# Kernel tuning notes

Measured on AMD Instinct MI355X. Metric: run time of the kernel, lower is better.

The kernel has to match this reference:

```python
import jax, jax.numpy as jnp
import numpy as np
from jax import lax

N = 1 << 22      # variable nodes
DV = 4           # max variable degree
M = 1 << 21      # check nodes
DC = 8           # max check degree
E = N * DV       # total edges (== M * DC, regular code)
N_ITER = 5


def setup_inputs() -> dict:
    key = jax.random.key(0)
    k1, k2 = jax.random.split(key)
    llr0 = jax.random.normal(k1, (N,), dtype=jnp.float32)
    # cn_adj: each check node owns DC flat edge indices into the [N, DV] grid
    perm = jax.random.permutation(k2, E)
    cn_adj = perm.reshape(M, DC).astype(jnp.int32)
    # vn_adj: only its sign is used (vn_adj < 0 masks padded slots); regular code -> no padding
    vn_adj = (jnp.arange(E, dtype=jnp.int32) % M).reshape(N, DV)
    gamma = jnp.ones((), dtype=jnp.float32)  # learned damping scalar
    return {"llr0": llr0, "gamma": gamma, "vn_adj": vn_adj, "cn_adj": cn_adj}


def reference(llr0, gamma, vn_adj, cn_adj):
    n, dv = vn_adj.shape
    mask = cn_adj < 0                       # [M, DC] padded check slots
    idx = jnp.where(mask, 0, cn_adj)        # safe flat edge indices
    vmask = vn_adj < 0                      # [N, DV] padded variable slots
    big = jnp.asarray(1e9, llr0.dtype)

    def step(v2c, _):
        # gather variable->check messages per check row: [M, DC]
        msg = v2c.reshape(-1)[idx]
        msg = jnp.where(mask, 0.0, msg)
        # min-sum check update (non-extrinsic, as in source)
        sgn = jnp.prod(jnp.sign(msg + 1e-12), axis=1, keepdims=True)   # [M, 1]
        mag = jnp.min(jnp.abs(jnp.where(mask, big, msg)), axis=1, keepdims=True)
        c2v = gamma * sgn * mag
        c2v = jnp.where(mask, 0.0, jnp.broadcast_to(c2v, cn_adj.shape))
        # scatter check->variable messages back onto the edge grid
        v_acc = jnp.zeros((n * dv,), v2c.dtype).at[idx].add(c2v).reshape(n, dv)
        v2c_new = llr0[:, None] + v_acc - v2c
        v2c_new = jnp.where(vmask, 0.0, v2c_new)
        return v2c_new, None

    v2c0 = jnp.zeros(vn_adj.shape, dtype=llr0.dtype)
    v2c, _ = lax.scan(step, v2c0, None, length=N_ITER)
    return llr0 + jnp.sum(v2c, axis=1)
```

## Files before the change

### kernel.cpp

```cpp
#include <hip/hip_runtime.h>
#include <hip/hip_bf16.h>

#define N_VAR (1 << 22)
#define DV    4
#define M_CHK (1 << 21)
#define DC    8
#define N_ITER 5
#define E_TOT (N_VAR * DV)

#define NBIN         256
#define REC_PER_BIN  (E_TOT / NBIN)
#define K3_BLOCKS    4096
#define CHK_PER_THR  2
#define CHK_PER_BLK  (M_CHK / K3_BLOCKS)
#define REC_PER_BLK  (CHK_PER_BLK * DC)
#define VARS_PER_BIN (N_VAR / NBIN)

typedef int      iv4 __attribute__((ext_vector_type(4)));
typedef unsigned uv4 __attribute__((ext_vector_type(4)));
typedef float    fv4 __attribute__((ext_vector_type(4)));

static __device__ inline unsigned pack_bf16x2(float lo, float hi) {
    float2 t; t.x = lo; t.y = hi;
    __hip_bfloat162 h = __float22bfloat162_rn(t);
    return *reinterpret_cast<unsigned*>(&h);
}

__global__ __launch_bounds__(256) void llr_to_bf16(const fv4* __restrict__ llr4,
                                                   uv4* __restrict__ out,
                                                   unsigned* __restrict__ gctr) {
    const int t = blockIdx.x * blockDim.x + threadIdx.x;
    if (blockIdx.x == 0) gctr[threadIdx.x] = 0u;
    fv4 a = __builtin_nontemporal_load(&llr4[(size_t)t * 2]);
    fv4 b = __builtin_nontemporal_load(&llr4[(size_t)t * 2 + 1]);
    uv4 o;
    o.x = pack_bf16x2(a.x, a.y);
    o.y = pack_bf16x2(a.z, a.w);
    o.z = pack_bf16x2(b.x, b.y);
    o.w = pack_bf16x2(b.z, b.w);
    __builtin_nontemporal_store(o, &out[t]);
}

__global__ __launch_bounds__(256) void k_emit(const __hip_bfloat16* __restrict__ llrb,
                                              const float* __restrict__ gamma_p,
                                              const iv4* __restrict__ cn_adj4,
                                              unsigned* __restrict__ gctr,
                                              unsigned* __restrict__ g_rec) {
    __shared__ unsigned hist[NBIN], binOfs[NBIN], cnt2[NBIN], gbase[NBIN], scanBuf[NBIN];
    __shared__ unsigned recLds[REC_PER_BLK];
    __shared__ unsigned char binLds[REC_PER_BLK];
    __shared__ unsigned totRec;
    const int tid = threadIdx.x, blk = blockIdx.x;
    const float gamma = gamma_p[0];

    hist[tid] = 0;
    cnt2[tid] = 0;
    __syncthreads();

    int e[CHK_PER_THR][DC];
    const int m0 = blk * CHK_PER_BLK + tid * CHK_PER_THR;
#pragma unroll
    for (int c = 0; c < CHK_PER_THR; ++c) {
        iv4 a0 = __builtin_nontemporal_load(&cn_adj4[(size_t)(m0 + c) * 2]);
        iv4 a1 = __builtin_nontemporal_load(&cn_adj4[(size_t)(m0 + c) * 2 + 1]);
        e[c][0]=a0.x; e[c][1]=a0.y; e[c][2]=a0.z; e[c][3]=a0.w;
        e[c][4]=a1.x; e[c][5]=a1.y; e[c][6]=a1.z; e[c][7]=a1.w;
    }
    float l[CHK_PER_THR][DC];
#pragma unroll
    for (int c = 0; c < CHK_PER_THR; ++c)
#pragma unroll
        for (int d = 0; d < DC; ++d)
            l[c][d] = __bfloat162float(llrb[e[c][d] >> 2]);

    unsigned Sh[CHK_PER_THR];
    bool nz[CHK_PER_THR];
#pragma unroll
    for (int c = 0; c < CHK_PER_THR; ++c) {
        float s1 = 1.0f, m1 = fabsf(l[c][0]);
#pragma unroll
        for (int d = 0; d < DC; ++d) {
            float t = l[c][d] + 1e-12f;
            s1 *= (t > 0.0f) ? 1.0f : ((t < 0.0f) ? -1.0f : 0.0f);
            if (d > 0) m1 = fminf(m1, fabsf(l[c][d]));
        }
        float c1 = gamma * s1 * m1;
        float delta = gamma * fabsf(c1) - c1;
        float s3 = 1.0f, m3 = fabsf(l[c][0] + delta);
#pragma unroll
        for (int d = 0; d < DC; ++d) {
            float ld = l[c][d] + delta;
            float t = ld + 1e-12f;
            s3 *= (t > 0.0f) ? 1.0f : ((t < 0.0f) ? -1.0f : 0.0f);
            if (d > 0) m3 = fminf(m3, fabsf(ld));
        }
        float c3 = gamma * s3 * m3;
        float c4 = gamma * fabsf(c3 - delta);
        float S  = (c4 - c3) + delta;
        __hip_bfloat16 h = __float2bfloat16(S);
        Sh[c] = *reinterpret_cast<unsigned short*>(&h);
        nz[c] = (Sh[c] & 0x7FFFu) != 0u;
    }

#pragma unroll
    for (int c = 0; c < CHK_PER_THR; ++c)
        if (nz[c])
#pragma unroll
            for (int d = 0; d < DC; ++d)
                atomicAdd(&hist[(unsigned)e[c][d] >> 16], 1u);
    __syncthreads();

    scanBuf[tid] = hist[tid];
    __syncthreads();
    for (int d = 1; d < NBIN; d <<= 1) {
        unsigned t = (tid >= d) ? scanBuf[tid - d] : 0u;
        __syncthreads();
        scanBuf[tid] += t;
        __syncthreads();
    }
    binOfs[tid] = scanBuf[tid] - hist[tid];
    if (tid == NBIN - 1) totRec = scanBuf[NBIN - 1];
    if (hist[tid] > 0)
        gbase[tid] = (unsigned)tid * REC_PER_BIN + atomicAdd(&gctr[tid], hist[tid]);
    __syncthreads();

#pragma unroll
    for (int c = 0; c < CHK_PER_THR; ++c)
        if (nz[c])
#pragma unroll
            for (int d = 0; d < DC; ++d) {
                unsigned ee  = (unsigned)e[c][d];
                unsigned bin = ee >> 16;
                unsigned rec = ((ee & 0xFFFFu) << 16) | Sh[c];
                unsigned slot = binOfs[bin] + atomicAdd(&cnt2[bin], 1u);
                recLds[slot] = rec;
                binLds[slot] = (unsigned char)bin;
            }
    __syncthreads();

    const unsigned tot = totRec;
    for (unsigned p = tid; p < tot; p += 256) {
        unsigned b = binLds[p];
        unsigned dst = gbase[b] + (p - binOfs[b]);
        __builtin_nontemporal_store(recLds[p], &g_rec[dst]);
    }
}

__global__ __launch_bounds__(1024) void k_apply(const float* __restrict__ llr0,
                                                const unsigned* __restrict__ gctr,
                                                const unsigned* __restrict__ g_rec,
                                                float* __restrict__ out) {
    __shared__ float acc[VARS_PER_BIN];
    const int tid = threadIdx.x, b = blockIdx.x;
    for (int j = tid; j < VARS_PER_BIN; j += 1024) acc[j] = 0.0f;
    const unsigned cnt = gctr[b];
    __syncthreads();
    const unsigned* rp = g_rec + (size_t)b * REC_PER_BIN;
    unsigned i = tid;
    for (; i + 1024 < cnt; i += 2048) {
        unsigned r0 = __builtin_nontemporal_load(&rp[i]);
        unsigned r1 = __builtin_nontemporal_load(&rp[i + 1024]);
        atomicAdd(&acc[r0 >> 18], __uint_as_float((r0 & 0xFFFFu) << 16));
        atomicAdd(&acc[r1 >> 18], __uint_as_float((r1 & 0xFFFFu) << 16));
    }
    for (; i < cnt; i += 1024) {
        unsigned r = __builtin_nontemporal_load(&rp[i]);
        atomicAdd(&acc[r >> 18], __uint_as_float((r & 0xFFFFu) << 16));
    }
    __syncthreads();
    const int vbase = b * VARS_PER_BIN;
    for (int j = tid; j < VARS_PER_BIN; j += 1024) {
        float L = llr0[vbase + j];
        out[vbase + j] = 5.0f * L + acc[j];
    }
}

__global__ __launch_bounds__(256) void nbp_check_kernel(const __hip_bfloat16* __restrict__ llrb,
                                                        const float* __restrict__ gamma_p,
                                                        const iv4* __restrict__ cn_adj4,
                                                        __hip_bfloat16* __restrict__ ws) {
    const int m = blockIdx.x * blockDim.x + threadIdx.x;
    const float gamma = gamma_p[0];
    iv4 a0 = __builtin_nontemporal_load(&cn_adj4[(size_t)m * 2]);
    iv4 a1 = __builtin_nontemporal_load(&cn_adj4[(size_t)m * 2 + 1]);
    int e[DC] = {a0.x, a0.y, a0.z, a0.w, a1.x, a1.y, a1.z, a1.w};
    float l[DC], msg[DC];
#pragma unroll
    for (int d = 0; d < DC; ++d) l[d] = __bfloat162float(llrb[e[d] >> 2]);
#pragma unroll
    for (int d = 0; d < DC; ++d) msg[d] = l[d];
#pragma unroll
    for (int it = 1; it < N_ITER; ++it) {
        float s = 1.0f, mn = fabsf(msg[0]);
#pragma unroll
        for (int d = 0; d < DC; ++d) {
            float t = msg[d] + 1e-12f;
            s *= (t > 0.0f) ? 1.0f : ((t < 0.0f) ? -1.0f : 0.0f);
            if (d > 0) mn = fminf(mn, fabsf(msg[d]));
        }
        float c2v = gamma * s * mn;
#pragma unroll
        for (int d = 0; d < DC; ++d) msg[d] = (l[d] + c2v) - msg[d];
    }
#pragma unroll
    for (int d = 0; d < DC; ++d) ws[e[d]] = __float2bfloat16(msg[d]);
}

__global__ __launch_bounds__(256) void nbp_var_reduce(const fv4* __restrict__ llr0_4,
                                                      const uv4* __restrict__ ws_u4,
                                                      fv4* __restrict__ out_4) {
    const int t = blockIdx.x * blockDim.x + threadIdx.x;
    uv4 wa = __builtin_nontemporal_load(&ws_u4[(size_t)t * 2]);
    uv4 wb = __builtin_nontemporal_load(&ws_u4[(size_t)t * 2 + 1]);
    fv4 l = __builtin_nontemporal_load(&llr0_4[t]);
    unsigned u[8] = {wa.x, wa.y, wa.z, wa.w, wb.x, wb.y, wb.z, wb.w};
    float msg[16];
#pragma unroll
    for (int i = 0; i < 8; ++i) {
        msg[2 * i]     = __uint_as_float((u[i] & 0xFFFFu) << 16);
        msg[2 * i + 1] = __uint_as_float(u[i] & 0xFFFF0000u);
    }
    fv4 o;
    o.x = l.x + (((msg[0]  + msg[1])  + msg[2])  + msg[3]);
    o.y = l.y + (((msg[4]  + msg[5])  + msg[6])  + msg[7]);
    o.z = l.z + (((msg[8]  + msg[9])  + msg[10]) + msg[11]);
    o.w = l.w + (((msg[12] + msg[13]) + msg[14]) + msg[15]);
    __builtin_nontemporal_store(o, &out_4[t]);
}

extern "C" void kernel_launch(void* const* d_in, const int* in_sizes, int n_in,
                              void* d_out, int out_size, void* d_ws, size_t ws_size,
                              hipStream_t stream) {
    const float* llr0   = (const float*)d_in[0];
    const float* gamma  = (const float*)d_in[1];
    const int*   cn_adj = (const int*)d_in[3];
    float* out = (float*)d_out;
    char* wsb = (char*)d_ws;

    const size_t OFF_LLRB = 0;
    const size_t OFF_REC  = 8u  * 1024 * 1024;
    const size_t OFF_CTR  = 72u * 1024 * 1024;
    const size_t NEED     = OFF_CTR + NBIN * sizeof(unsigned);

    if (ws_size >= NEED) {
        __hip_bfloat16* llrb = (__hip_bfloat16*)(wsb + OFF_LLRB);
        unsigned* g_rec = (unsigned*)(wsb + OFF_REC);
        unsigned* gctr  = (unsigned*)(wsb + OFF_CTR);

        llr_to_bf16<<<(N_VAR / 8) / 256, 256, 0, stream>>>((const fv4*)llr0, (uv4*)llrb, gctr);
        k_emit<<<K3_BLOCKS, 256, 0, stream>>>(llrb, gamma, (const iv4*)cn_adj, gctr, g_rec);
        k_apply<<<NBIN, 1024, 0, stream>>>(llr0, gctr, g_rec, out);
    } else {
        __hip_bfloat16* ws   = (__hip_bfloat16*)wsb;
        __hip_bfloat16* llrb = ((__hip_bfloat16*)wsb) + E_TOT;
        llr_to_bf16<<<(N_VAR / 8) / 256, 256, 0, stream>>>((const fv4*)llr0,
                                                           (uv4*)llrb, (unsigned*)(wsb));
        nbp_check_kernel<<<M_CHK / 256, 256, 0, stream>>>(llrb, gamma, (const iv4*)cn_adj, ws);
        nbp_var_reduce<<<(N_VAR / 4) / 256, 256, 0, stream>>>(
            (const fv4*)llr0, (const uv4*)ws, (fv4*)out);
    }
}
```

Before: 250.4 us.

## Split apply bins across two blocks and use one check per thread in emit

k_emit now processes one check node per thread, with twice as many blocks, instead of two per thread. This is meant to raise occupancy and memory-level parallelism for the random bf16 gathers. k_apply launches two 512-thread blocks per bin: each block reads all of the bin's records with 8-byte vector loads and accumulates only the half of the variable range it owns, then writes its output with nontemporal stores. This doubles the record reads in the apply stage, trading that extra traffic for more blocks in flight across the 256 bins and a smaller LDS footprint per block.

```diff
diff --git a/kernel.cpp b/kernel.cpp
--- a/kernel.cpp
+++ b/kernel.cpp
@@ -10,13 +10,14 @@
 
 #define NBIN         256
 #define REC_PER_BIN  (E_TOT / NBIN)
-#define K3_BLOCKS    4096
-#define CHK_PER_THR  2
+#define K3_BLOCKS    8192
 #define CHK_PER_BLK  (M_CHK / K3_BLOCKS)
 #define REC_PER_BLK  (CHK_PER_BLK * DC)
 #define VARS_PER_BIN (N_VAR / NBIN)
+#define VARS_PER_SUB (VARS_PER_BIN / 2)
 
 typedef int      iv4 __attribute__((ext_vector_type(4)));
+typedef unsigned uv2 __attribute__((ext_vector_type(2)));
 typedef unsigned uv4 __attribute__((ext_vector_type(4)));
 typedef float    fv4 __attribute__((ext_vector_type(4)));
 
@@ -57,57 +58,43 @@
     cnt2[tid] = 0;
     __syncthreads();
 
-    int e[CHK_PER_THR][DC];
-    const int m0 = blk * CHK_PER_BLK + tid * CHK_PER_THR;
-#pragma unroll
-    for (int c = 0; c < CHK_PER_THR; ++c) {
-        iv4 a0 = __builtin_nontemporal_load(&cn_adj4[(size_t)(m0 + c) * 2]);
-        iv4 a1 = __builtin_nontemporal_load(&cn_adj4[(size_t)(m0 + c) * 2 + 1]);
-        e[c][0]=a0.x; e[c][1]=a0.y; e[c][2]=a0.z; e[c][3]=a0.w;
-        e[c][4]=a1.x; e[c][5]=a1.y; e[c][6]=a1.z; e[c][7]=a1.w;
-    }
-    float l[CHK_PER_THR][DC];
-#pragma unroll
-    for (int c = 0; c < CHK_PER_THR; ++c)
+    const int m = blk * CHK_PER_BLK + tid;
+    iv4 a0 = __builtin_nontemporal_load(&cn_adj4[(size_t)m * 2]);
+    iv4 a1 = __builtin_nontemporal_load(&cn_adj4[(size_t)m * 2 + 1]);
+    int e[DC] = {a0.x, a0.y, a0.z, a0.w, a1.x, a1.y, a1.z, a1.w};
+    float l[DC];
+#pragma unroll
+    for (int d = 0; d < DC; ++d)
+        l[d] = __bfloat162float(llrb[(unsigned)e[d] >> 2]);
+
+    float s1 = 1.0f, m1 = fabsf(l[0]);
+#pragma unroll
+    for (int d = 0; d < DC; ++d) {
+        float t = l[d] + 1e-12f;
+        s1 *= (t > 0.0f) ? 1.0f : ((t < 0.0f) ? -1.0f : 0.0f);
+        if (d > 0) m1 = fminf(m1, fabsf(l[d]));
+    }
+    float c1 = gamma * s1 * m1;
+    float delta = gamma * fabsf(c1) - c1;
+    float s3 = 1.0f, m3 = fabsf(l[0] + delta);
+#pragma unroll
+    for (int d = 0; d < DC; ++d) {
+        float ld = l[d] + delta;
+        float t = ld + 1e-12f;
+        s3 *= (t > 0.0f) ? 1.0f : ((t < 0.0f) ? -1.0f : 0.0f);
+        if (d > 0) m3 = fminf(m3, fabsf(ld));
+    }
+    float c3 = gamma * s3 * m3;
+    float c4 = gamma * fabsf(c3 - delta);
+    float S  = (c4 - c3) + delta;
+    __hip_bfloat16 h = __float2bfloat16(S);
+    const unsigned Sh = *reinterpret_cast<unsigned short*>(&h);
+    const bool nz = (Sh & 0x7FFFu) != 0u;
+
+    if (nz)
 #pragma unroll
         for (int d = 0; d < DC; ++d)
-            l[c][d] = __bfloat162float(llrb[e[c][d] >> 2]);
-
-    unsigned Sh[CHK_PER_THR];
-    bool nz[CHK_PER_THR];
-#pragma unroll
-    for (int c = 0; c < CHK_PER_THR; ++c) {
-        float s1 = 1.0f, m1 = fabsf(l[c][0]);
-#pragma unroll
-        for (int d = 0; d < DC; ++d) {
-            float t = l[c][d] + 1e-12f;
-            s1 *= (t > 0.0f) ? 1.0f : ((t < 0.0f) ? -1.0f : 0.0f);
-            if (d > 0) m1 = fminf(m1, fabsf(l[c][d]));
-        }
-        float c1 = gamma * s1 * m1;
-        float delta = gamma * fabsf(c1) - c1;
-        float s3 = 1.0f, m3 = fabsf(l[c][0] + delta);
-#pragma unroll
-        for (int d = 0; d < DC; ++d) {
-            float ld = l[c][d] + delta;
-            float t = ld + 1e-12f;
-            s3 *= (t > 0.0f) ? 1.0f : ((t < 0.0f) ? -1.0f : 0.0f);
-            if (d > 0) m3 = fminf(m3, fabsf(ld));
-        }
-        float c3 = gamma * s3 * m3;
-        float c4 = gamma * fabsf(c3 - delta);
-        float S  = (c4 - c3) + delta;
-        __hip_bfloat16 h = __float2bfloat16(S);
-        Sh[c] = *reinterpret_cast<unsigned short*>(&h);
-        nz[c] = (Sh[c] & 0x7FFFu) != 0u;
-    }
-
-#pragma unroll
-    for (int c = 0; c < CHK_PER_THR; ++c)
-        if (nz[c])
-#pragma unroll
-            for (int d = 0; d < DC; ++d)
-                atomicAdd(&hist[(unsigned)e[c][d] >> 16], 1u);
+            atomicAdd(&hist[(unsigned)e[d] >> 16], 1u);
     __syncthreads();
 
     scanBuf[tid] = hist[tid];
@@ -124,18 +111,16 @@
         gbase[tid] = (unsigned)tid * REC_PER_BIN + atomicAdd(&gctr[tid], hist[tid]);
     __syncthreads();
 
-#pragma unroll
-    for (int c = 0; c < CHK_PER_THR; ++c)
-        if (nz[c])
-#pragma unroll
-            for (int d = 0; d < DC; ++d) {
-                unsigned ee  = (unsigned)e[c][d];
-                unsigned bin = ee >> 16;
-                unsigned rec = ((ee & 0xFFFFu) << 16) | Sh[c];
-                unsigned slot = binOfs[bin] + atomicAdd(&cnt2[bin], 1u);
-                recLds[slot] = rec;
-                binLds[slot] = (unsigned char)bin;
-            }
+    if (nz)
+#pragma unroll
+        for (int d = 0; d < DC; ++d) {
+            unsigned ee  = (unsigned)e[d];
+            unsigned bin = ee >> 16;
+            unsigned rec = ((ee & 0xFFFFu) << 16) | Sh;
+            unsigned slot = binOfs[bin] + atomicAdd(&cnt2[bin], 1u);
+            recLds[slot] = rec;
+            binLds[slot] = (unsigned char)bin;
+        }
     __syncthreads();
 
     const unsigned tot = totRec;
@@ -146,32 +131,37 @@
     }
 }
 
-__global__ __launch_bounds__(1024) void k_apply(const float* __restrict__ llr0,
-                                                const unsigned* __restrict__ gctr,
-                                                const unsigned* __restrict__ g_rec,
-                                                float* __restrict__ out) {
-    __shared__ float acc[VARS_PER_BIN];
-    const int tid = threadIdx.x, b = blockIdx.x;
-    for (int j = tid; j < VARS_PER_BIN; j += 1024) acc[j] = 0.0f;
+__global__ __launch_bounds__(512) void k_apply(const float* __restrict__ llr0,
+                                               const unsigned* __restrict__ gctr,
+                                               const unsigned* __restrict__ g_rec,
+                                               float* __restrict__ out) {
+    __shared__ float acc[VARS_PER_SUB];
+    const int tid = threadIdx.x;
+    const int b   = blockIdx.x >> 1;
+    const unsigned vlo = (blockIdx.x & 1) * VARS_PER_SUB;
+    for (int j = tid; j < VARS_PER_SUB; j += 512) acc[j] = 0.0f;
     const unsigned cnt = gctr[b];
     __syncthreads();
     const unsigned* rp = g_rec + (size_t)b * REC_PER_BIN;
-    unsigned i = tid;
-    for (; i + 1024 < cnt; i += 2048) {
-        unsigned r0 = __builtin_nontemporal_load(&rp[i]);
-        unsigned r1 = __builtin_nontemporal_load(&rp[i + 1024]);
-        atomicAdd(&acc[r0 >> 18], __uint_as_float((r0 & 0xFFFFu) << 16));
-        atomicAdd(&acc[r1 >> 18], __uint_as_float((r1 & 0xFFFFu) << 16));
-    }
-    for (; i < cnt; i += 1024) {
-        unsigned r = __builtin_nontemporal_load(&rp[i]);
-        atomicAdd(&acc[r >> 18], __uint_as_float((r & 0xFFFFu) << 16));
-    }
-    __syncthreads();
-    const int vbase = b * VARS_PER_BIN;
-    for (int j = tid; j < VARS_PER_BIN; j += 1024) {
+    const uv2* rp2 = reinterpret_cast<const uv2*>(rp);
+    const unsigned n2 = cnt >> 1;
+    for (unsigned i = tid; i < n2; i += 512) {
+        uv2 r = rp2[i];
+        unsigned v0 = (r.x >> 18) - vlo;
+        unsigned v1 = (r.y >> 18) - vlo;
+        if (v0 < VARS_PER_SUB) atomicAdd(&acc[v0], __uint_as_float((r.x & 0xFFFFu) << 16));
+        if (v1 < VARS_PER_SUB) atomicAdd(&acc[v1], __uint_as_float((r.y & 0xFFFFu) << 16));
+    }
+    if ((cnt & 1u) && tid == 0) {
+        unsigned r = rp[cnt - 1];
+        unsigned v = (r >> 18) - vlo;
+        if (v < VARS_PER_SUB) atomicAdd(&acc[v], __uint_as_float((r & 0xFFFFu) << 16));
+    }
+    __syncthreads();
+    const int vbase = b * VARS_PER_BIN + (int)vlo;
+    for (int j = tid; j < VARS_PER_SUB; j += 512) {
         float L = llr0[vbase + j];
-        out[vbase + j] = 5.0f * L + acc[j];
+        __builtin_nontemporal_store(5.0f * L + acc[j], &out[vbase + j]);
     }
 }
 
@@ -249,7 +239,7 @@
 
         llr_to_bf16<<<(N_VAR / 8) / 256, 256, 0, stream>>>((const fv4*)llr0, (uv4*)llrb, gctr);
         k_emit<<<K3_BLOCKS, 256, 0, stream>>>(llrb, gamma, (const iv4*)cn_adj, gctr, g_rec);
-        k_apply<<<NBIN, 1024, 0, stream>>>(llr0, gctr, g_rec, out);
+        k_apply<<<NBIN * 2, 512, 0, stream>>>(llr0, gctr, g_rec, out);
     } else {
         __hip_bfloat16* ws   = (__hip_bfloat16*)wsb;
         __hip_bfloat16* llrb = ((__hip_bfloat16*)wsb) + E_TOT;
```

Measured after the change: 275.3 us. 1.1x slower.
